# Performance work log

Measured on AMD Instinct MI355X. Metric: run time of the kernel, lower is better.

## Reference

```python
import jax, jax.numpy as jnp
import numpy as np

MAX_DIST = 50.0
NO_NEIGHBORS = 0.0
# feature order: [dx, dy, size_a, size_b, angle]; angle mark is cyclic
FEATURES_RANGE = np.array([50.0, 50.0, 32.0, 32.0, np.pi], dtype=np.float32)
FEATURES_CYCLIC = np.array([False, False, False, False, True])


def setup_inputs() -> dict:
    key = jax.random.key(0)
    ks = jax.random.split(key, 8)
    B, N, M, F, H = 8, 1024, 1024, 5, 4
    points = jax.random.normal(ks[0], (B, N, F), jnp.float32)
    context_points = jax.random.normal(ks[1], (B, M, F), jnp.float32)
    points_mask = jnp.ones((B, N), dtype=bool)
    context_points_mask = jnp.ones((B, M), dtype=bool)
    distance_matrix = jax.random.uniform(ks[2], (B, N, M), jnp.float32) * 100.0
    interactions_mask = jax.random.randint(ks[3], (B, N, M), 0, 2).astype(bool)
    # q_fun MLP: Linear(5,4) -> ReLU -> Linear(4,1) -> Sigmoid
    W1 = jax.random.normal(ks[4], (F, H), jnp.float32) / np.sqrt(F)
    b1 = jnp.zeros((H,), jnp.float32)
    W2 = jax.random.normal(ks[5], (H, 1), jnp.float32) / np.sqrt(H)
    b2 = jnp.zeros((1,), jnp.float32)
    # attention weight model: Linear(5,1)
    Wa = jax.random.normal(ks[6], (F, 1), jnp.float32) / np.sqrt(F)
    ba = jnp.zeros((1,), jnp.float32)
    return dict(points=points, points_mask=points_mask,
                context_points=context_points, context_points_mask=context_points_mask,
                distance_matrix=distance_matrix, interactions_mask=interactions_mask,
                global_max_dist=100,
                W1=W1, b1=b1, W2=W2, b2=b2, Wa=Wa, ba=ba)


def reference(points, points_mask, context_points, context_points_mask,
              distance_matrix, interactions_mask, global_max_dist,
              W1, b1, W2, b2, Wa, ba):
    fr = jnp.asarray(FEATURES_RANGE)
    cyc = jnp.asarray(FEATURES_CYCLIC)
    # pairwise abs feature differences: [B, N, M, 5]
    fd = jnp.abs(points[:, :, None, :] - context_points[:, None, :, :])
    fn = fd / fr
    fc = jnp.remainder(fn, 1.0)
    fc = jnp.minimum(fc, 1.0 - fc)           # cyclic wrap-around distance
    fn = jnp.where(cyc, fc, fn)
    # q_fun MLP + sigmoid -> per-pair similarity energy [B, N, M]
    h = jax.nn.relu(jnp.einsum('bnmf,fh->bnmh', fn, W1) + b1)
    energy = jax.nn.sigmoid(jnp.einsum('bnmh,ho->bnmo', h, W2) + b2)[..., 0]
    # interaction mask, tightened by max_dist when max_dist < global_max_dist
    ib = interactions_mask
    if MAX_DIST < global_max_dist:
        ib = ib & (distance_matrix <= MAX_DIST)
    # masked attention reduce over context axis (dim 2)
    scores = (jnp.einsum('bnmf,fo->bnmo', fn, Wa) + ba)[..., 0]
    scores = jnp.where(ib, scores, -jnp.inf)
    weights = jax.nn.softmax(scores, axis=2)  # all-masked rows -> NaN
    reduced = jnp.sum(weights * energy, axis=2)
    reduced = jnp.nan_to_num(reduced, nan=NO_NEIGHBORS,
                             posinf=NO_NEIGHBORS, neginf=NO_NEIGHBORS)
    return reduced
```

## Files before the change

kernel.cpp:

```cpp
#include <hip/hip_runtime.h>
#include <math.h>

#define BATCH   8
#define NPTS    1024
#define MCTX    1024
#define BN      (BATCH * NPTS)

#define INV_R0  0.02f
#define INV_R1  0.02f
#define INV_R2  0.03125f
#define INV_R3  0.03125f
#define INV_PI  0.3183098861837907f
#define MAX_DIST 50.0f
#define LOG2E   1.4426950408889634f

__global__ __launch_bounds__(256, 8) void sim_kernel(
    const float* __restrict__ points,
    const float* __restrict__ ctx,
    const float* __restrict__ dist,
    const unsigned char* __restrict__ imask,
    const int* __restrict__ gmd_p,
    const float* __restrict__ W1p,
    const float* __restrict__ b1p,
    const float* __restrict__ W2p,
    const float* __restrict__ b2p,
    const float* __restrict__ Wap,
    const float* __restrict__ bap,
    float* __restrict__ out)
{
    __shared__ unsigned short q[4][MCTX];

    const int wid  = threadIdx.x >> 6;
    const int lane = threadIdx.x & 63;
    const int row  = __builtin_amdgcn_readfirstlane((int)blockIdx.x * 4 + wid);
    const int b    = row >> 10;

    const float4*       __restrict__ d4  = (const float4*)(dist + (size_t)row * MCTX);
    const unsigned int* __restrict__ m4p = (const unsigned int*)(imask + (size_t)row * MCTX);
    const float4 dv0 = d4[lane],       dv1 = d4[lane + 64],
                 dv2 = d4[lane + 128], dv3 = d4[lane + 192];
    const unsigned int mv0 = m4p[lane],       mv1 = m4p[lane + 64],
                       mv2 = m4p[lane + 128], mv3 = m4p[lane + 192];

    const float p0 = points[row*5+0], p1 = points[row*5+1], p2 = points[row*5+2],
                p3 = points[row*5+3], p4 = points[row*5+4];
    float w1[20];
#pragma unroll
    for (int i = 0; i < 20; ++i) w1[i] = W1p[i];
    float b1v[4];
#pragma unroll
    for (int j = 0; j < 4; ++j) b1v[j] = b1p[j];
    float w2[4];
#pragma unroll
    for (int j = 0; j < 4; ++j) w2[j] = W2p[j];
    const float b2v = b2p[0];
    float wa[5];
#pragma unroll
    for (int f = 0; f < 5; ++f) wa[f] = Wap[f];
    const float bav = bap[0];
    const bool tighten = (MAX_DIST < (float)gmd_p[0]);

    unsigned okbits = 0;
    {
        const float4 dvv[4] = { dv0, dv1, dv2, dv3 };
        const unsigned int mvv[4] = { mv0, mv1, mv2, mv3 };
#pragma unroll
        for (int j = 0; j < 4; ++j) {
            const float dd[4] = { dvv[j].x, dvv[j].y, dvv[j].z, dvv[j].w };
#pragma unroll
            for (int t = 0; t < 4; ++t) {
                bool ok = ((mvv[j] >> (8*t)) & 0xFFu) != 0u;
                if (tighten) ok = ok && (dd[t] <= MAX_DIST);
                okbits |= ok ? (1u << (4*j + t)) : 0u;
            }
        }
    }

    int tot = 0;
#pragma unroll
    for (int k = 0; k < 16; ++k) {
        const bool ok = (okbits >> k) & 1u;
        unsigned long long bm = __ballot(ok);
        unsigned rank = __builtin_amdgcn_mbcnt_hi(
                            (unsigned)(bm >> 32),
                            __builtin_amdgcn_mbcnt_lo((unsigned)bm, 0u));
        if (ok) {
            const int m = (lane + 64 * (k >> 2)) * 4 + (k & 3);
            q[wid][tot + rank] = (unsigned short)m;
        }
        tot += (int)__popcll(bm);
    }

    const float* __restrict__ cb = ctx + (size_t)b * MCTX * 5;
    float lsum = 0.0f, asum = 0.0f;
#pragma unroll 2
    for (int i = lane; i < tot; i += 64) {
        const int m = (int)q[wid][i];
        const float* __restrict__ c = cb + m * 5;
        const float c0 = c[0], c1 = c[1], c2 = c[2], c3 = c[3], c4 = c[4];

        const float a0 = fabsf(p0 - c0) * INV_R0;
        const float a1 = fabsf(p1 - c1) * INV_R1;
        const float a2 = fabsf(p2 - c2) * INV_R2;
        const float a3 = fabsf(p3 - c3) * INV_R3;
        float g   = __builtin_amdgcn_fractf(fabsf(p4 - c4) * INV_PI);
        float fn4 = fminf(g, 1.0f - g);

        float h0 = fmaxf(0.0f, b1v[0] + a0*w1[0] + a1*w1[4] + a2*w1[8]  + a3*w1[12] + fn4*w1[16]);
        float h1 = fmaxf(0.0f, b1v[1] + a0*w1[1] + a1*w1[5] + a2*w1[9]  + a3*w1[13] + fn4*w1[17]);
        float h2 = fmaxf(0.0f, b1v[2] + a0*w1[2] + a1*w1[6] + a2*w1[10] + a3*w1[14] + fn4*w1[18]);
        float h3 = fmaxf(0.0f, b1v[3] + a0*w1[3] + a1*w1[7] + a2*w1[11] + a3*w1[15] + fn4*w1[19]);

        float z  = b2v + h0*w2[0] + h1*w2[1] + h2*w2[2] + h3*w2[3];
        float energy = __builtin_amdgcn_rcpf(1.0f + __builtin_amdgcn_exp2f(z * (-LOG2E)));

        float score = bav + a0*wa[0] + a1*wa[1] + a2*wa[2] + a3*wa[3] + fn4*wa[4];
        float e  = __builtin_amdgcn_exp2f(score * LOG2E);

        lsum += e;
        asum = fmaf(e, energy, asum);
    }

#pragma unroll
    for (int off = 1; off < 64; off <<= 1) {
        lsum += __shfl_xor(lsum, off, 64);
        asum += __shfl_xor(asum, off, 64);
    }

    if (lane == 0) {
        out[row] = (lsum > 0.0f) ? (asum / lsum) : 0.0f;
    }
}

extern "C" void kernel_launch(void* const* d_in, const int* in_sizes, int n_in,
                              void* d_out, int out_size, void* d_ws, size_t ws_size,
                              hipStream_t stream) {
    const float*         points = (const float*)d_in[0];
    const float*         ctx    = (const float*)d_in[2];
    const float*         dist   = (const float*)d_in[4];
    const unsigned char* imask  = (const unsigned char*)d_in[5];
    const int*           gmd    = (const int*)d_in[6];
    const float*         W1     = (const float*)d_in[7];
    const float*         b1     = (const float*)d_in[8];
    const float*         W2     = (const float*)d_in[9];
    const float*         b2     = (const float*)d_in[10];
    const float*         Wa     = (const float*)d_in[11];
    const float*         ba     = (const float*)d_in[12];
    float*               out    = (float*)d_out;

    dim3 block(256);
    dim3 grid(BN / 4);
    sim_kernel<<<grid, block, 0, stream>>>(points, ctx, dist, imask, gmd,
                                           W1, b1, W2, b2, Wa, ba, out);
}
```

Baseline: 16.25 us.

## Interleave mask compaction with per-chunk compute to overlap loads and math

```diff
diff --git a/kernel.cpp b/kernel.cpp
--- a/kernel.cpp
+++ b/kernel.cpp
@@ -37,10 +37,14 @@
 
     const float4*       __restrict__ d4  = (const float4*)(dist + (size_t)row * MCTX);
     const unsigned int* __restrict__ m4p = (const unsigned int*)(imask + (size_t)row * MCTX);
-    const float4 dv0 = d4[lane],       dv1 = d4[lane + 64],
-                 dv2 = d4[lane + 128], dv3 = d4[lane + 192];
-    const unsigned int mv0 = m4p[lane],       mv1 = m4p[lane + 64],
-                       mv2 = m4p[lane + 128], mv3 = m4p[lane + 192];
+    const float4       dv0 = d4[lane];
+    const unsigned int mv0 = m4p[lane];
+    const float4       dv1 = d4[lane + 64];
+    const unsigned int mv1 = m4p[lane + 64];
+    const float4       dv2 = d4[lane + 128];
+    const unsigned int mv2 = m4p[lane + 128];
+    const float4       dv3 = d4[lane + 192];
+    const unsigned int mv3 = m4p[lane + 192];
 
     const float p0 = points[row*5+0], p1 = points[row*5+1], p2 = points[row*5+2],
                 p3 = points[row*5+3], p4 = points[row*5+4];
@@ -60,41 +64,13 @@
     const float bav = bap[0];
     const bool tighten = (MAX_DIST < (float)gmd_p[0]);
 
-    unsigned okbits = 0;
-    {
-        const float4 dvv[4] = { dv0, dv1, dv2, dv3 };
-        const unsigned int mvv[4] = { mv0, mv1, mv2, mv3 };
-#pragma unroll
-        for (int j = 0; j < 4; ++j) {
-            const float dd[4] = { dvv[j].x, dvv[j].y, dvv[j].z, dvv[j].w };
-#pragma unroll
-            for (int t = 0; t < 4; ++t) {
-                bool ok = ((mvv[j] >> (8*t)) & 0xFFu) != 0u;
-                if (tighten) ok = ok && (dd[t] <= MAX_DIST);
-                okbits |= ok ? (1u << (4*j + t)) : 0u;
-            }
-        }
-    }
+    const float* __restrict__ cb = ctx + (size_t)b * MCTX * 5;
 
-    int tot = 0;
-#pragma unroll
-    for (int k = 0; k < 16; ++k) {
-        const bool ok = (okbits >> k) & 1u;
-        unsigned long long bm = __ballot(ok);
-        unsigned rank = __builtin_amdgcn_mbcnt_hi(
-                            (unsigned)(bm >> 32),
-                            __builtin_amdgcn_mbcnt_lo((unsigned)bm, 0u));
-        if (ok) {
-            const int m = (lane + 64 * (k >> 2)) * 4 + (k & 3);
-            q[wid][tot + rank] = (unsigned short)m;
-        }
-        tot += (int)__popcll(bm);
-    }
+    int   tot  = 0;
+    int   done = 0;
+    float lsum = 0.0f, asum = 0.0f;
 
-    const float* __restrict__ cb = ctx + (size_t)b * MCTX * 5;
-    float lsum = 0.0f, asum = 0.0f;
-#pragma unroll 2
-    for (int i = lane; i < tot; i += 64) {
+    auto body = [&](int i) {
         const int m = (int)q[wid][i];
         const float* __restrict__ c = cb + m * 5;
         const float c0 = c[0], c1 = c[1], c2 = c[2], c3 = c[3], c4 = c[4];
@@ -111,15 +87,44 @@
         float h2 = fmaxf(0.0f, b1v[2] + a0*w1[2] + a1*w1[6] + a2*w1[10] + a3*w1[14] + fn4*w1[18]);
         float h3 = fmaxf(0.0f, b1v[3] + a0*w1[3] + a1*w1[7] + a2*w1[11] + a3*w1[15] + fn4*w1[19]);
 
-        float z  = b2v + h0*w2[0] + h1*w2[1] + h2*w2[2] + h3*w2[3];
+        float z      = b2v + h0*w2[0] + h1*w2[1] + h2*w2[2] + h3*w2[3];
         float energy = __builtin_amdgcn_rcpf(1.0f + __builtin_amdgcn_exp2f(z * (-LOG2E)));
 
         float score = bav + a0*wa[0] + a1*wa[1] + a2*wa[2] + a3*wa[3] + fn4*wa[4];
-        float e  = __builtin_amdgcn_exp2f(score * LOG2E);
+        float e     = __builtin_amdgcn_exp2f(score * LOG2E);
 
         lsum += e;
         asum = fmaf(e, energy, asum);
-    }
+    };
+
+    auto stage = [&](const float4& dv, unsigned int mv, int jbase) {
+        const float dd[4] = { dv.x, dv.y, dv.z, dv.w };
+#pragma unroll
+        for (int t = 0; t < 4; ++t) {
+            bool ok = ((mv >> (8*t)) & 0xFFu) != 0u;
+            if (tighten) ok = ok && (dd[t] <= MAX_DIST);
+            unsigned long long bm = __ballot(ok);
+            unsigned rank = __builtin_amdgcn_mbcnt_hi(
+                                (unsigned)(bm >> 32),
+                                __builtin_amdgcn_mbcnt_lo((unsigned)bm, 0u));
+            if (ok) {
+                const int m = (lane + 64 * jbase) * 4 + t;
+                q[wid][tot + rank] = (unsigned short)m;
+            }
+            tot += (int)__popcll(bm);
+        }
+        while (tot - done >= 64) {
+            body(done + lane);
+            done += 64;
+        }
+    };
+
+    stage(dv0, mv0, 0);
+    stage(dv1, mv1, 1);
+    stage(dv2, mv2, 2);
+    stage(dv3, mv3, 3);
+
+    if (done + lane < tot) body(done + lane);
 
 #pragma unroll
     for (int off = 1; off < 64; off <<= 1) {
```

Result: faster. 15.36 us (-5.5%).
